# Kernel optimization log

Hardware: AMD Instinct MI355X
Metric: run time of the kernel (lower is better)

The kernel has to match this reference:

```python
import jax, jax.numpy as jnp
import numpy as np

THETA = 10000.0
R_TOK = 4  # region_token_num


def _local_positions(regions, max_n):
    # 0-based position of each token within its region (count of prior tokens
    # with the same region id) -- order-based, works for any region layout.
    onehot = jax.nn.one_hot(regions, max_n + 1, dtype=jnp.int32)  # [B,T,N+1]
    counts = jnp.cumsum(onehot, axis=1)                            # inclusive
    return jnp.take_along_axis(counts, regions[..., None], axis=-1)[..., 0] - 1


def _rope(q, k, pos, theta):
    # full-head-dim rotary embedding, split-half convention
    D = q.shape[-1]
    inv_freq = 1.0 / (theta ** (jnp.arange(0, D, 2, dtype=jnp.float32) / D))  # [D/2]
    ang = pos[..., None].astype(jnp.float32) * inv_freq                        # [B,S,D/2]
    cos = jnp.tile(jnp.cos(ang), (1, 1, 2))[:, None]                           # [B,1,S,D]
    sin = jnp.tile(jnp.sin(ang), (1, 1, 2))[:, None]

    def rot(x):
        h = x.shape[-1] // 2
        return jnp.concatenate([-x[..., h:], x[..., :h]], axis=-1)

    return q * cos + rot(q) * sin, k * cos + rot(k) * sin


def setup_inputs() -> dict:
    B, H, D = 2, 16, 64
    T, MAX_N = 2048, 64
    P = MAX_N * R_TOK
    key = jax.random.key(0)
    ks = jax.random.split(key, 7)
    f = lambda k, s: jax.random.normal(k, s, dtype=jnp.float32)
    regions = jnp.sort(jax.random.randint(ks[6], (B, T), 1, MAX_N + 1, dtype=jnp.int32), axis=-1)
    return {
        'pool_q': f(ks[0], (B, H, P, D)),
        'pool_k': f(ks[1], (B, H, P, D)),
        'pool_v': f(ks[2], (B, H, P, D)),
        'x_q': f(ks[3], (B, H, T, D)),
        'x_k': f(ks[4], (B, H, T, D)),
        'x_v': f(ks[5], (B, H, T, D)),
        'regions': regions,
        't_mask': jnp.ones((B, T), dtype=bool),
        'n_mask': jnp.ones((B, MAX_N), dtype=bool),
        'max_n': MAX_N,
    }


def reference(pool_q, pool_k, pool_v, x_q, x_k, x_v, regions, t_mask, n_mask, max_n):
    B, H, P, D = pool_q.shape
    R = R_TOK
    # sequence = [pool, x]
    q = jnp.concatenate([pool_q, x_q], axis=2)
    k = jnp.concatenate([pool_k, x_k], axis=2)
    v = jnp.concatenate([pool_v, x_v], axis=2)

    # local-mode positions (use_pool_offset=False -> pool tokens at pos 0)
    pool_pos = jnp.zeros((B, P), dtype=jnp.int32)
    x_pos = (_local_positions(regions, max_n) + R) * (regions > 0).astype(jnp.int32)
    pos = jnp.concatenate([pool_pos, x_pos], axis=-1)  # [B,S]
    q, k = _rope(q, k, pos, THETA)

    # block-local (same-region) mask: [B,1,S,S], True = allowed
    pool_region = jnp.broadcast_to(jnp.repeat(jnp.arange(1, max_n + 1, dtype=jnp.int32), R)[None], (B, P))
    pool_valid = jnp.repeat(n_mask, R, axis=1)                      # [B,P]
    full_region = jnp.concatenate([pool_region, regions], axis=-1)  # [B,S]
    full_valid = jnp.concatenate([pool_valid, t_mask], axis=-1)     # [B,S]
    same = full_region[:, :, None] == full_region[:, None, :]
    valid = full_valid[:, :, None] & full_valid[:, None, :]
    nonpad = (full_region != 0)[:, :, None] & (full_region != 0)[:, None, :]
    mask = (same & valid & nonpad)[:, None]                          # [B,1,S,S]

    scores = jnp.einsum('bhqd,bhkd->bhqk', q, k) / jnp.sqrt(jnp.float32(D))
    scores = jnp.where(mask, scores, jnp.float32(-1e9))
    attn = jax.nn.softmax(scores, axis=-1)
    out = jnp.einsum('bhqk,bhkd->bhqd', attn, v)
    return out[:, :, :P, :]
```

## Files before the change

### kernel.cpp

```cpp
#include <hip/hip_runtime.h>

#define BB   2
#define HH   16
#define DD   64
#define TT   2048
#define MAXN 64
#define RTOK 4
#define PP   (MAXN * RTOK)
#define SPAD 72

typedef unsigned short u16x8 __attribute__((ext_vector_type(8)));
typedef unsigned short u16x4 __attribute__((ext_vector_type(4)));

__device__ __forceinline__ unsigned short f2bf(float f) {
    unsigned u = __float_as_uint(f);
    u += 0x7FFFu + ((u >> 16) & 1u);
    return (unsigned short)(u >> 16);
}
__device__ __forceinline__ float bf2f(unsigned short u) {
    return __uint_as_float(((unsigned int)u) << 16);
}

__global__ __launch_bounds__(256)
void build_ranges(const int* __restrict__ regions, int* __restrict__ tab) {
    const int b   = blockIdx.x;
    const int tid = threadIdx.x;
    const int* reg = regions + b * TT;
    int* t = tab + b * 66;
    const int i0 = tid * 8;
    int v[9];
    const int4 a0 = *(const int4*)(reg + i0);
    const int4 a1 = *(const int4*)(reg + i0 + 4);
    v[0] = a0.x; v[1] = a0.y; v[2] = a0.z; v[3] = a0.w;
    v[4] = a1.x; v[5] = a1.y; v[6] = a1.z; v[7] = a1.w;
    v[8] = (tid == 255) ? (MAXN + 1) : reg[i0 + 8];
    if (tid == 0)
        for (int rr = 1; rr <= v[0]; ++rr) t[rr] = 0;
    #pragma unroll
    for (int j = 0; j < 8; ++j)
        for (int rr = v[j] + 1; rr <= v[j + 1]; ++rr) t[rr] = i0 + j + 1;
}

__global__ __launch_bounds__(256, 6)
void lapd_attn(const float* __restrict__ pool_q,
               const float* __restrict__ pool_k,
               const float* __restrict__ pool_v,
               const float* __restrict__ x_k,
               const float* __restrict__ x_v,
               const int* __restrict__ tab,
               float* __restrict__ out) {
    const int blk   = blockIdx.x;
    const int r_idx = blk & (MAXN - 1);
    const int bh    = blk >> 6;
    const int b     = bh / HH;

    const int tid  = threadIdx.x;
    const int wave = tid >> 6;
    const int lane = tid & 63;

    __shared__ __align__(16) unsigned short k_s16[64][SPAD];
    __shared__ __align__(16) unsigned short v_t16[64][SPAD];
    __shared__ float q_s[4][DD];
    __shared__ float p_s[4][64];

    const size_t poolbase = ((size_t)bh * PP + r_idx * RTOK) * DD;
    const float* pk = pool_k + poolbase;
    const float* pv = pool_v + poolbase;
    const float* xk = x_k + (size_t)bh * TT * DD;
    const float* xv = x_v + (size_t)bh * TT * DD;

    const size_t qidx = poolbase + (size_t)(wave * DD) + lane;
    q_s[wave][lane] = pool_q[qidx] * 0.125f;

    const int* tb    = tab + b * 66;
    const int start  = tb[r_idx + 1];
    const int cnt    = tb[r_idx + 2] - start;
    const int sstart = (cnt > 0) ? start : 0;

    const int g = tid >> 3;
    const int d = (tid & 7) * 4;

    float invf[4];
    #pragma unroll
    for (int c = 0; c < 4; ++c)
        invf[c] = __expf((float)(d + c) * (-9.210340371976184f / 32.0f));

    float acc = 0.0f, l = 0.0f;
    int xbase = 0;
    bool first = true;

    for (;;) {
        const int koff = first ? RTOK : 0;
        int nx = cnt - xbase;
        if (nx > 64 - koff) nx = 64 - koff;
        if (nx < 0) nx = 0;
        const int tn = koff + nx;

        float4 kA0, kA1, vA0, vA1, kB0, kB1, vB0, vB1;
        int xiA, xiB;
        bool poolA, poolB;
        {
            const int keyA = 2 * g;
            xiA = keyA - koff; if (xiA > nx - 1) xiA = nx - 1; if (xiA < 0) xiA = 0;
            poolA = first && (keyA < RTOK);
            const float* kb = poolA ? (pk + keyA * DD)
                                    : (xk + (size_t)(sstart + xbase + xiA) * DD);
            const float* vb = poolA ? (pv + keyA * DD)
                                    : (xv + (size_t)(sstart + xbase + xiA) * DD);
            kA0 = *(const float4*)(kb + d);
            kA1 = *(const float4*)(kb + d + 32);
            vA0 = *(const float4*)(vb + d);
            vA1 = *(const float4*)(vb + d + 32);
        }
        {
            const int keyB = 2 * g + 1;
            xiB = keyB - koff; if (xiB > nx - 1) xiB = nx - 1; if (xiB < 0) xiB = 0;
            poolB = first && (keyB < RTOK);
            const float* kb = poolB ? (pk + keyB * DD)
                                    : (xk + (size_t)(sstart + xbase + xiB) * DD);
            const float* vb = poolB ? (pv + keyB * DD)
                                    : (xv + (size_t)(sstart + xbase + xiB) * DD);
            kB0 = *(const float4*)(kb + d);
            kB1 = *(const float4*)(kb + d + 32);
            vB0 = *(const float4*)(vb + d);
            vB1 = *(const float4*)(vb + d + 32);
        }

        {
            float lo[4] = {kA0.x, kA0.y, kA0.z, kA0.w};
            float hi[4] = {kA1.x, kA1.y, kA1.z, kA1.w};
            if (!poolA) {
                const float pos = (float)(xbase + xiA + RTOK);
                #pragma unroll
                for (int c = 0; c < 4; ++c) {
                    float sv, cv;
                    __sincosf(pos * invf[c], &sv, &cv);
                    const float L = lo[c], H = hi[c];
                    lo[c] = L * cv - H * sv;
                    hi[c] = H * cv + L * sv;
                }
            }
            u16x4 wlo = {f2bf(lo[0]), f2bf(lo[1]), f2bf(lo[2]), f2bf(lo[3])};
            u16x4 whi = {f2bf(hi[0]), f2bf(hi[1]), f2bf(hi[2]), f2bf(hi[3])};
            *(u16x4*)&k_s16[2 * g][d]      = wlo;
            *(u16x4*)&k_s16[2 * g][d + 32] = whi;
        }
        {
            float lo[4] = {kB0.x, kB0.y, kB0.z, kB0.w};
            float hi[4] = {kB1.x, kB1.y, kB1.z, kB1.w};
            if (!poolB) {
                const float pos = (float)(xbase + xiB + RTOK);
                #pragma unroll
                for (int c = 0; c < 4; ++c) {
                    float sv, cv;
                    __sincosf(pos * invf[c], &sv, &cv);
                    const float L = lo[c], H = hi[c];
                    lo[c] = L * cv - H * sv;
                    hi[c] = H * cv + L * sv;
                }
            }
            u16x4 wlo = {f2bf(lo[0]), f2bf(lo[1]), f2bf(lo[2]), f2bf(lo[3])};
            u16x4 whi = {f2bf(hi[0]), f2bf(hi[1]), f2bf(hi[2]), f2bf(hi[3])};
            *(u16x4*)&k_s16[2 * g + 1][d]      = wlo;
            *(u16x4*)&k_s16[2 * g + 1][d + 32] = whi;
        }
        {
            const float a0[4] = {vA0.x, vA0.y, vA0.z, vA0.w};
            const float a1[4] = {vA1.x, vA1.y, vA1.z, vA1.w};
            const float b0[4] = {vB0.x, vB0.y, vB0.z, vB0.w};
            const float b1[4] = {vB1.x, vB1.y, vB1.z, vB1.w};
            #pragma unroll
            for (int c = 0; c < 4; ++c) {
                const unsigned plo = (unsigned)f2bf(a0[c]) | ((unsigned)f2bf(b0[c]) << 16);
                const unsigned phi = (unsigned)f2bf(a1[c]) | ((unsigned)f2bf(b1[c]) << 16);
                *(unsigned*)&v_t16[d + c][2 * g]      = plo;
                *(unsigned*)&v_t16[d + 32 + c][2 * g] = phi;
            }
        }
        __syncthreads();

        float s0 = 0, s1 = 0, s2 = 0, s3 = 0;
        #pragma unroll
        for (int dd2 = 0; dd2 < DD; dd2 += 8) {
            const u16x8 kk = *(const u16x8*)&k_s16[lane][dd2];
            const float4 qa = *(const float4*)&q_s[wave][dd2];
            const float4 qb = *(const float4*)&q_s[wave][dd2 + 4];
            s0 += qa.x * bf2f(kk[0]) + qb.x * bf2f(kk[4]);
            s1 += qa.y * bf2f(kk[1]) + qb.y * bf2f(kk[5]);
            s2 += qa.z * bf2f(kk[2]) + qb.z * bf2f(kk[6]);
            s3 += qa.w * bf2f(kk[3]) + qb.w * bf2f(kk[7]);
        }
        const float s = (s0 + s1) + (s2 + s3);
        p_s[wave][lane] = (lane < tn) ? __expf(s) : 0.0f;

        float a0 = 0, a1 = 0, a2 = 0, a3 = 0, l0 = 0;
        #pragma unroll
        for (int k = 0; k < 64; k += 8) {
            const u16x8 vv = *(const u16x8*)&v_t16[lane][k];
            const float4 pa = *(const float4*)&p_s[wave][k];
            const float4 pb = *(const float4*)&p_s[wave][k + 4];
            a0 += pa.x * bf2f(vv[0]) + pb.x * bf2f(vv[4]);
            a1 += pa.y * bf2f(vv[1]) + pb.y * bf2f(vv[5]);
            a2 += pa.z * bf2f(vv[2]) + pb.z * bf2f(vv[6]);
            a3 += pa.w * bf2f(vv[3]) + pb.w * bf2f(vv[7]);
            l0 += (pa.x + pa.y + pa.z + pa.w) + (pb.x + pb.y + pb.z + pb.w);
        }
        acc += (a0 + a1) + (a2 + a3);
        l   += l0;

        xbase += nx;
        first = false;
        if (xbase >= cnt) break;
        __syncthreads();
    }

    out[qidx] = acc / l;
}

extern "C" void kernel_launch(void* const* d_in, const int* in_sizes, int n_in,
                              void* d_out, int out_size, void* d_ws, size_t ws_size,
                              hipStream_t stream) {
    const float* pool_q  = (const float*)d_in[0];
    const float* pool_k  = (const float*)d_in[1];
    const float* pool_v  = (const float*)d_in[2];
    const float* x_k     = (const float*)d_in[4];
    const float* x_v     = (const float*)d_in[5];
    const int*   regions = (const int*)d_in[6];
    float*       out     = (float*)d_out;
    int*         tab     = (int*)d_ws;

    build_ranges<<<dim3(BB), dim3(256), 0, stream>>>(regions, tab);
    lapd_attn<<<dim3(BB * HH * MAXN), dim3(256), 0, stream>>>(
        pool_q, pool_k, pool_v, x_k, x_v, tab, out);
}
```

Before: 119.8 us.

## Use one wavefront per region block instead of four waves

```diff
diff --git a/kernel.cpp b/kernel.cpp
--- a/kernel.cpp
+++ b/kernel.cpp
@@ -7,7 +7,7 @@
 #define MAXN 64
 #define RTOK 4
 #define PP   (MAXN * RTOK)
-#define SPAD 72
+#define STR  72
 
 typedef unsigned short u16x8 __attribute__((ext_vector_type(8)));
 typedef unsigned short u16x4 __attribute__((ext_vector_type(4)));
@@ -41,7 +41,7 @@
         for (int rr = v[j] + 1; rr <= v[j + 1]; ++rr) t[rr] = i0 + j + 1;
 }
 
-__global__ __launch_bounds__(256, 6)
+__global__ __launch_bounds__(64, 2)
 void lapd_attn(const float* __restrict__ pool_q,
                const float* __restrict__ pool_k,
                const float* __restrict__ pool_v,
@@ -53,15 +53,17 @@
     const int r_idx = blk & (MAXN - 1);
     const int bh    = blk >> 6;
     const int b     = bh / HH;
-
-    const int tid  = threadIdx.x;
-    const int wave = tid >> 6;
-    const int lane = tid & 63;
-
-    __shared__ __align__(16) unsigned short k_s16[64][SPAD];
-    __shared__ __align__(16) unsigned short v_t16[64][SPAD];
+    const int lane  = threadIdx.x;
+
+    __shared__ __align__(16) unsigned short k_s16[64][STR];
+    __shared__ __align__(16) unsigned short v_t16[64][STR];
+    __shared__ __align__(16) unsigned short p_s16[4][STR];
     __shared__ float q_s[4][DD];
-    __shared__ float p_s[4][64];
+
+    const int* tb    = tab + b * 66;
+    const int start  = tb[r_idx + 1];
+    const int cnt    = tb[r_idx + 2] - start;
+    const int sstart = (cnt > 0) ? start : 0;
 
     const size_t poolbase = ((size_t)bh * PP + r_idx * RTOK) * DD;
     const float* pk = pool_k + poolbase;
@@ -69,23 +71,22 @@
     const float* xk = x_k + (size_t)bh * TT * DD;
     const float* xv = x_v + (size_t)bh * TT * DD;
 
-    const size_t qidx = poolbase + (size_t)(wave * DD) + lane;
-    q_s[wave][lane] = pool_q[qidx] * 0.125f;
-
-    const int* tb    = tab + b * 66;
-    const int start  = tb[r_idx + 1];
-    const int cnt    = tb[r_idx + 2] - start;
-    const int sstart = (cnt > 0) ? start : 0;
-
-    const int g = tid >> 3;
-    const int d = (tid & 7) * 4;
-
+    const int qr = lane >> 4;
+    const int qc = (lane & 15) * 4;
+    {
+        const float4 q4 = *(const float4*)(pool_q + poolbase + (size_t)(qr * DD) + qc);
+        *(float4*)&q_s[qr][qc] =
+            make_float4(q4.x * 0.125f, q4.y * 0.125f, q4.z * 0.125f, q4.w * 0.125f);
+    }
+
+    const int g = lane >> 3;
+    const int d = (lane & 7) * 4;
     float invf[4];
     #pragma unroll
     for (int c = 0; c < 4; ++c)
         invf[c] = __expf((float)(d + c) * (-9.210340371976184f / 32.0f));
 
-    float acc = 0.0f, l = 0.0f;
+    float a0 = 0, a1 = 0, a2 = 0, a3 = 0, l = 0;
     int xbase = 0;
     bool first = true;
 
@@ -96,85 +97,86 @@
         if (nx < 0) nx = 0;
         const int tn = koff + nx;
 
-        float4 kA0, kA1, vA0, vA1, kB0, kB1, vB0, vB1;
-        int xiA, xiB;
-        bool poolA, poolB;
-        {
-            const int keyA = 2 * g;
-            xiA = keyA - koff; if (xiA > nx - 1) xiA = nx - 1; if (xiA < 0) xiA = 0;
-            poolA = first && (keyA < RTOK);
-            const float* kb = poolA ? (pk + keyA * DD)
-                                    : (xk + (size_t)(sstart + xbase + xiA) * DD);
-            const float* vb = poolA ? (pv + keyA * DD)
-                                    : (xv + (size_t)(sstart + xbase + xiA) * DD);
-            kA0 = *(const float4*)(kb + d);
-            kA1 = *(const float4*)(kb + d + 32);
-            vA0 = *(const float4*)(vb + d);
-            vA1 = *(const float4*)(vb + d + 32);
-        }
-        {
-            const int keyB = 2 * g + 1;
-            xiB = keyB - koff; if (xiB > nx - 1) xiB = nx - 1; if (xiB < 0) xiB = 0;
-            poolB = first && (keyB < RTOK);
-            const float* kb = poolB ? (pk + keyB * DD)
-                                    : (xk + (size_t)(sstart + xbase + xiB) * DD);
-            const float* vb = poolB ? (pv + keyB * DD)
-                                    : (xv + (size_t)(sstart + xbase + xiB) * DD);
-            kB0 = *(const float4*)(kb + d);
-            kB1 = *(const float4*)(kb + d + 32);
-            vB0 = *(const float4*)(vb + d);
-            vB1 = *(const float4*)(vb + d + 32);
-        }
-
-        {
-            float lo[4] = {kA0.x, kA0.y, kA0.z, kA0.w};
-            float hi[4] = {kA1.x, kA1.y, kA1.z, kA1.w};
-            if (!poolA) {
-                const float pos = (float)(xbase + xiA + RTOK);
-                #pragma unroll
-                for (int c = 0; c < 4; ++c) {
+        __syncthreads();
+
+        #pragma unroll
+        for (int ph = 0; ph < 4; ++ph) {
+            const int keyA = ph * 16 + 2 * g;
+            const int keyB = keyA + 1;
+            int xiA = keyA - koff; if (xiA > nx - 1) xiA = nx - 1; if (xiA < 0) xiA = 0;
+            int xiB = keyB - koff; if (xiB > nx - 1) xiB = nx - 1; if (xiB < 0) xiB = 0;
+            const bool pA = first && (keyA < RTOK);
+            const bool pB = first && (keyB < RTOK);
+            const float* kbA = pA ? (pk + keyA * DD) : (xk + (size_t)(sstart + xbase + xiA) * DD);
+            const float* vbA = pA ? (pv + keyA * DD) : (xv + (size_t)(sstart + xbase + xiA) * DD);
+            const float* kbB = pB ? (pk + keyB * DD) : (xk + (size_t)(sstart + xbase + xiB) * DD);
+            const float* vbB = pB ? (pv + keyB * DD) : (xv + (size_t)(sstart + xbase + xiB) * DD);
+            const float4 kA0 = *(const float4*)(kbA + d);
+            const float4 kA1 = *(const float4*)(kbA + d + 32);
+            const float4 vA0 = *(const float4*)(vbA + d);
+            const float4 vA1 = *(const float4*)(vbA + d + 32);
+            const float4 kB0 = *(const float4*)(kbB + d);
+            const float4 kB1 = *(const float4*)(kbB + d + 32);
+            const float4 vB0 = *(const float4*)(vbB + d);
+            const float4 vB1 = *(const float4*)(vbB + d + 32);
+
+            {
+                float lo0 = kA0.x, lo1 = kA0.y, lo2 = kA0.z, lo3 = kA0.w;
+                float hi0 = kA1.x, hi1 = kA1.y, hi2 = kA1.z, hi3 = kA1.w;
+                if (!pA) {
+                    const float pos = (float)(xbase + xiA + RTOK);
                     float sv, cv;
-                    __sincosf(pos * invf[c], &sv, &cv);
-                    const float L = lo[c], H = hi[c];
-                    lo[c] = L * cv - H * sv;
-                    hi[c] = H * cv + L * sv;
+                    __sincosf(pos * invf[0], &sv, &cv);
+                    { const float L = lo0, H = hi0; lo0 = L*cv - H*sv; hi0 = H*cv + L*sv; }
+                    __sincosf(pos * invf[1], &sv, &cv);
+                    { const float L = lo1, H = hi1; lo1 = L*cv - H*sv; hi1 = H*cv + L*sv; }
+                    __sincosf(pos * invf[2], &sv, &cv);
+                    { const float L = lo2, H = hi2; lo2 = L*cv - H*sv; hi2 = H*cv + L*sv; }
+                    __sincosf(pos * invf[3], &sv, &cv);
+                    { const float L = lo3, H = hi3; lo3 = L*cv - H*sv; hi3 = H*cv + L*sv; }
                 }
+                u16x4 wlo = {f2bf(lo0), f2bf(lo1), f2bf(lo2), f2bf(lo3)};
+                u16x4 whi = {f2bf(hi0), f2bf(hi1), f2bf(hi2), f2bf(hi3)};
+                *(u16x4*)&k_s16[keyA][d]      = wlo;
+                *(u16x4*)&k_s16[keyA][d + 32] = whi;
             }
-            u16x4 wlo = {f2bf(lo[0]), f2bf(lo[1]), f2bf(lo[2]), f2bf(lo[3])};
-            u16x4 whi = {f2bf(hi[0]), f2bf(hi[1]), f2bf(hi[2]), f2bf(hi[3])};
-            *(u16x4*)&k_s16[2 * g][d]      = wlo;
-            *(u16x4*)&k_s16[2 * g][d + 32] = whi;
-        }
-        {
-            float lo[4] = {kB0.x, kB0.y, kB0.z, kB0.w};
-            float hi[4] = {kB1.x, kB1.y, kB1.z, kB1.w};
-            if (!poolB) {
-                const float pos = (float)(xbase + xiB + RTOK);
-                #pragma unroll
-                for (int c = 0; c < 4; ++c) {
+            {
+                float lo0 = kB0.x, lo1 = kB0.y, lo2 = kB0.z, lo3 = kB0.w;
+                float hi0 = kB1.x, hi1 = kB1.y, hi2 = kB1.z, hi3 = kB1.w;
+                if (!pB) {
+                    const float pos = (float)(xbase + xiB + RTOK);
                     float sv, cv;
-                    __sincosf(pos * invf[c], &sv, &cv);
-                    const float L = lo[c], H = hi[c];
-                    lo[c] = L * cv - H * sv;
-                    hi[c] = H * cv + L * sv;
+                    __sincosf(pos * invf[0], &sv, &cv);
+                    { const float L = lo0, H = hi0; lo0 = L*cv - H*sv; hi0 = H*cv + L*sv; }
+                    __sincosf(pos * invf[1], &sv, &cv);
+                    { const float L = lo1, H = hi1; lo1 = L*cv - H*sv; hi1 = H*cv + L*sv; }
+                    __sincosf(pos * invf[2], &sv, &cv);
+                    { const float L = lo2, H = hi2; lo2 = L*cv - H*sv; hi2 = H*cv + L*sv; }
+                    __sincosf(pos * invf[3], &sv, &cv);
+                    { const float L = lo3, H = hi3; lo3 = L*cv - H*sv; hi3 = H*cv + L*sv; }
                 }
+                u16x4 wlo = {f2bf(lo0), f2bf(lo1), f2bf(lo2), f2bf(lo3)};
+                u16x4 whi = {f2bf(hi0), f2bf(hi1), f2bf(hi2), f2bf(hi3)};
+                *(u16x4*)&k_s16[keyB][d]      = wlo;
+                *(u16x4*)&k_s16[keyB][d + 32] = whi;
             }
-            u16x4 wlo = {f2bf(lo[0]), f2bf(lo[1]), f2bf(lo[2]), f2bf(lo[3])};
-            u16x4 whi = {f2bf(hi[0]), f2bf(hi[1]), f2bf(hi[2]), f2bf(hi[3])};
-            *(u16x4*)&k_s16[2 * g + 1][d]      = wlo;
-            *(u16x4*)&k_s16[2 * g + 1][d + 32] = whi;
-        }
-        {
-            const float a0[4] = {vA0.x, vA0.y, vA0.z, vA0.w};
-            const float a1[4] = {vA1.x, vA1.y, vA1.z, vA1.w};
-            const float b0[4] = {vB0.x, vB0.y, vB0.z, vB0.w};
-            const float b1[4] = {vB1.x, vB1.y, vB1.z, vB1.w};
-            #pragma unroll
-            for (int c = 0; c < 4; ++c) {
-                const unsigned plo = (unsigned)f2bf(a0[c]) | ((unsigned)f2bf(b0[c]) << 16);
-                const unsigned phi = (unsigned)f2bf(a1[c]) | ((unsigned)f2bf(b1[c]) << 16);
-                *(unsigned*)&v_t16[d + c][2 * g]      = plo;
-                *(unsigned*)&v_t16[d + 32 + c][2 * g] = phi;
+            {
+                const unsigned w0 = (unsigned)f2bf(vA0.x) | ((unsigned)f2bf(vB0.x) << 16);
+                const unsigned w1 = (unsigned)f2bf(vA0.y) | ((unsigned)f2bf(vB0.y) << 16);
+                const unsigned w2 = (unsigned)f2bf(vA0.z) | ((unsigned)f2bf(vB0.z) << 16);
+                const unsigned w3 = (unsigned)f2bf(vA0.w) | ((unsigned)f2bf(vB0.w) << 16);
+                const unsigned h0 = (unsigned)f2bf(vA1.x) | ((unsigned)f2bf(vB1.x) << 16);
+                const unsigned h1 = (unsigned)f2bf(vA1.y) | ((unsigned)f2bf(vB1.y) << 16);
+                const unsigned h2 = (unsigned)f2bf(vA1.z) | ((unsigned)f2bf(vB1.z) << 16);
+                const unsigned h3 = (unsigned)f2bf(vA1.w) | ((unsigned)f2bf(vB1.w) << 16);
+                *(unsigned*)&v_t16[d + 0][keyA]      = w0;
+                *(unsigned*)&v_t16[d + 1][keyA]      = w1;
+                *(unsigned*)&v_t16[d + 2][keyA]      = w2;
+                *(unsigned*)&v_t16[d + 3][keyA]      = w3;
+                *(unsigned*)&v_t16[d + 32][keyA]     = h0;
+                *(unsigned*)&v_t16[d + 33][keyA]     = h1;
+                *(unsigned*)&v_t16[d + 34][keyA]     = h2;
+                *(unsigned*)&v_t16[d + 35][keyA]     = h3;
             }
         }
         __syncthreads();
@@ -183,38 +185,56 @@
         #pragma unroll
         for (int dd2 = 0; dd2 < DD; dd2 += 8) {
             const u16x8 kk = *(const u16x8*)&k_s16[lane][dd2];
-            const float4 qa = *(const float4*)&q_s[wave][dd2];
-            const float4 qb = *(const float4*)&q_s[wave][dd2 + 4];
-            s0 += qa.x * bf2f(kk[0]) + qb.x * bf2f(kk[4]);
-            s1 += qa.y * bf2f(kk[1]) + qb.y * bf2f(kk[5]);
-            s2 += qa.z * bf2f(kk[2]) + qb.z * bf2f(kk[6]);
-            s3 += qa.w * bf2f(kk[3]) + qb.w * bf2f(kk[7]);
+            const float k0 = bf2f(kk[0]), k1 = bf2f(kk[1]), k2 = bf2f(kk[2]), k3 = bf2f(kk[3]);
+            const float k4 = bf2f(kk[4]), k5 = bf2f(kk[5]), k6 = bf2f(kk[6]), k7 = bf2f(kk[7]);
+            const float4 qa0 = *(const float4*)&q_s[0][dd2];
+            const float4 qb0 = *(const float4*)&q_s[0][dd2 + 4];
+            const float4 qa1 = *(const float4*)&q_s[1][dd2];
+            const float4 qb1 = *(const float4*)&q_s[1][dd2 + 4];
+            const float4 qa2 = *(const float4*)&q_s[2][dd2];
+            const float4 qb2 = *(const float4*)&q_s[2][dd2 + 4];
+            const float4 qa3 = *(const float4*)&q_s[3][dd2];
+            const float4 qb3 = *(const float4*)&q_s[3][dd2 + 4];
+            s0 += qa0.x*k0 + qa0.y*k1 + qa0.z*k2 + qa0.w*k3 + qb0.x*k4 + qb0.y*k5 + qb0.z*k6 + qb0.w*k7;
+            s1 += qa1.x*k0 + qa1.y*k1 + qa1.z*k2 + qa1.w*k3 + qb1.x*k4 + qb1.y*k5 + qb1.z*k6 + qb1.w*k7;
+            s2 += qa2.x*k0 + qa2.y*k1 + qa2.z*k2 + qa2.w*k3 + qb2.x*k4 + qb2.y*k5 + qb2.z*k6 + qb2.w*k7;
+            s3 += qa3.x*k0 + qa3.y*k1 + qa3.z*k2 + qa3.w*k3 + qb3.x*k4 + qb3.y*k5 + qb3.z*k6 + qb3.w*k7;
         }
-        const float s = (s0 + s1) + (s2 + s3);
-        p_s[wave][lane] = (lane < tn) ? __expf(s) : 0.0f;
-
-        float a0 = 0, a1 = 0, a2 = 0, a3 = 0, l0 = 0;
+        const bool ok = (lane < tn);
+        p_s16[0][lane] = f2bf(ok ? __expf(s0) : 0.0f);
+        p_s16[1][lane] = f2bf(ok ? __expf(s1) : 0.0f);
+        p_s16[2][lane] = f2bf(ok ? __expf(s2) : 0.0f);
+        p_s16[3][lane] = f2bf(ok ? __expf(s3) : 0.0f);
+        __syncthreads();
+
         #pragma unroll
         for (int k = 0; k < 64; k += 8) {
-            const u16x8 vv = *(const u16x8*)&v_t16[lane][k];
-            const float4 pa = *(const float4*)&p_s[wave][k];
-            const float4 pb = *(const float4*)&p_s[wave][k + 4];
-            a0 += pa.x * bf2f(vv[0]) + pb.x * bf2f(vv[4]);
-            a1 += pa.y * bf2f(vv[1]) + pb.y * bf2f(vv[5]);
-            a2 += pa.z * bf2f(vv[2]) + pb.z * bf2f(vv[6]);
-            a3 += pa.w * bf2f(vv[3]) + pb.w * bf2f(vv[7]);
-            l0 += (pa.x + pa.y + pa.z + pa.w) + (pb.x + pb.y + pb.z + pb.w);
+            const u16x8 pp = *(const u16x8*)&p_s16[qr][k];
+            const float p0 = bf2f(pp[0]), p1 = bf2f(pp[1]), p2 = bf2f(pp[2]), p3 = bf2f(pp[3]);
+            const float p4 = bf2f(pp[4]), p5 = bf2f(pp[5]), p6 = bf2f(pp[6]), p7 = bf2f(pp[7]);
+            const u16x8 w0 = *(const u16x8*)&v_t16[qc + 0][k];
+            const u16x8 w1 = *(const u16x8*)&v_t16[qc + 1][k];
+            const u16x8 w2 = *(const u16x8*)&v_t16[qc + 2][k];
+            const u16x8 w3 = *(const u16x8*)&v_t16[qc + 3][k];
+            a0 += p0*bf2f(w0[0]) + p1*bf2f(w0[1]) + p2*bf2f(w0[2]) + p3*bf2f(w0[3])
+                + p4*bf2f(w0[4]) + p5*bf2f(w0[5]) + p6*bf2f(w0[6]) + p7*bf2f(w0[7]);
+            a1 += p0*bf2f(w1[0]) + p1*bf2f(w1[1]) + p2*bf2f(w1[2]) + p3*bf2f(w1[3])
+                + p4*bf2f(w1[4]) + p5*bf2f(w1[5]) + p6*bf2f(w1[6]) + p7*bf2f(w1[7]);
+            a2 += p0*bf2f(w2[0]) + p1*bf2f(w2[1]) + p2*bf2f(w2[2]) + p3*bf2f(w2[3])
+                + p4*bf2f(w2[4]) + p5*bf2f(w2[5]) + p6*bf2f(w2[6]) + p7*bf2f(w2[7]);
+            a3 += p0*bf2f(w3[0]) + p1*bf2f(w3[1]) + p2*bf2f(w3[2]) + p3*bf2f(w3[3])
+                + p4*bf2f(w3[4]) + p5*bf2f(w3[5]) + p6*bf2f(w3[6]) + p7*bf2f(w3[7]);
+            l  += ((p0 + p1) + (p2 + p3)) + ((p4 + p5) + (p6 + p7));
         }
-        acc += (a0 + a1) + (a2 + a3);
-        l   += l0;
 
         xbase += nx;
         first = false;
         if (xbase >= cnt) break;
-        __syncthreads();
     }
 
-    out[qidx] = acc / l;
+    const float rl = 1.0f / l;
+    *(float4*)(out + poolbase + (size_t)(qr * DD) + qc) =
+        make_float4(a0 * rl, a1 * rl, a2 * rl, a3 * rl);
 }
 
 extern "C" void kernel_launch(void* const* d_in, const int* in_sizes, int n_in,
@@ -230,6 +250,6 @@
     int*         tab     = (int*)d_ws;
 
     build_ranges<<<dim3(BB), dim3(256), 0, stream>>>(regions, tab);
-    lapd_attn<<<dim3(BB * HH * MAXN), dim3(256), 0, stream>>>(
+    lapd_attn<<<dim3(BB * HH * MAXN), dim3(64), 0, stream>>>(
         pool_q, pool_k, pool_v, x_k, x_v, tab, out);
 }
```

Result: faster. 110.8 us (-7.5%).
